# Optimization experiments

Hardware: AMD Instinct MI355X
Metric: run time of the kernel (lower is better)

Reference implementation:

```python
import jax, jax.numpy as jnp
import numpy as np

N = 50000          # nodes
E = 800000         # edges per metapath
M = 3              # metapaths
IN_DIM = 256
H = 8              # heads
D = 32             # out_dim per head
HID = 128          # semantic attention hidden
NEG_SLOPE = 0.2    # DGL GATConv default leaky_relu slope


def setup_inputs() -> dict:
    key = jax.random.key(0)
    ks = jax.random.split(key, 10)
    h = jax.random.normal(ks[0], (N, IN_DIM), dtype=jnp.float32)
    src = jax.random.randint(ks[1], (M, E), 0, N, dtype=jnp.int32)
    dst = jax.random.randint(ks[2], (M, E), 0, N, dtype=jnp.int32)
    s = 1.0 / np.sqrt(IN_DIM)
    fc_w = jax.random.normal(ks[3], (M, IN_DIM, H * D), dtype=jnp.float32) * s
    attn_l = jax.random.normal(ks[4], (M, H, D), dtype=jnp.float32) * 0.1
    attn_r = jax.random.normal(ks[5], (M, H, D), dtype=jnp.float32) * 0.1
    bias = jnp.zeros((M, H * D), dtype=jnp.float32)
    sem_w1 = jax.random.normal(ks[6], (H * D, HID), dtype=jnp.float32) * (1.0 / np.sqrt(H * D))
    sem_b1 = jnp.zeros((HID,), dtype=jnp.float32)
    sem_w2 = jax.random.normal(ks[7], (HID, 1), dtype=jnp.float32) * (1.0 / np.sqrt(HID))
    return {"h": h, "src": src, "dst": dst, "fc_w": fc_w, "attn_l": attn_l,
            "attn_r": attn_r, "bias": bias, "sem_w1": sem_w1, "sem_b1": sem_b1,
            "sem_w2": sem_w2}


def _gat(h, src, dst, fc_w, attn_l, attn_r, bias):
    # DGL GATConv (eval mode, dropout=0), activation=elu.
    feat = (h @ fc_w).reshape(N, H, D)                       # [N,H,D]
    el = jnp.sum(feat * attn_l, axis=-1)                     # [N,H]
    er = jnp.sum(feat * attn_r, axis=-1)                     # [N,H]
    e = jax.nn.leaky_relu(el[src] + er[dst], NEG_SLOPE)      # [E,H]
    # edge softmax over incoming edges of each dst node
    emax = jax.ops.segment_max(e, dst, num_segments=N)       # [N,H]
    emax = jnp.where(jnp.isfinite(emax), emax, 0.0)
    ee = jnp.exp(e - emax[dst])                              # [E,H]
    esum = jax.ops.segment_sum(ee, dst, num_segments=N)      # [N,H]
    alpha = ee / jnp.maximum(esum[dst], 1e-38)               # [E,H]
    msg = feat[src] * alpha[:, :, None]                      # [E,H,D]
    rst = jax.ops.segment_sum(msg, dst, num_segments=N)      # [N,H,D]
    rst = rst + bias.reshape(1, H, D)
    return jax.nn.elu(rst).reshape(N, H * D)                 # flatten heads


def reference(h, src, dst, fc_w, attn_l, attn_r, bias, sem_w1, sem_b1, sem_w2):
    gat_all = jax.vmap(_gat, in_axes=(None, 0, 0, 0, 0, 0, 0))
    z_m = gat_all(h, src, dst, fc_w, attn_l, attn_r, bias)   # [M,N,F]
    z_m = jnp.transpose(z_m, (1, 0, 2))                      # [N,M,F]
    # semantic attention
    w = jnp.tanh(z_m @ sem_w1 + sem_b1) @ sem_w2             # [N,M,1]
    w = w.mean(axis=0)                                       # [M,1]
    a_w = jax.nn.softmax(w, axis=0)                          # [M,1]
    z = jnp.sum(z_m * a_w[None, :, :], axis=1)               # [N,F]
    return z
```

## Files before the change

kernel.cpp:

```cpp
#include <hip/hip_runtime.h>
#include <math.h>

#define NN   50000
#define EE   800000
#define MM   3
#define KDIM 256
#define FF   256
#define HH   8
#define DD   32
#define HID  128
#define SLOPE 0.2f
#define BK   32
#define CAP  80

typedef unsigned short u16;
typedef unsigned int   u32;
typedef __attribute__((ext_vector_type(8))) short short8;
typedef __attribute__((ext_vector_type(4))) float floatx4;

__device__ __forceinline__ float eluf(float x) { return x > 0.f ? x : expm1f(x); }

__device__ __forceinline__ float b2f_lo(u32 u) {
    union { u32 i; float f; } v; v.i = u << 16; return v.f;
}
__device__ __forceinline__ float b2f_hi(u32 u) {
    union { u32 i; float f; } v; v.i = u & 0xffff0000u; return v.f;
}
__device__ __forceinline__ u16 f2b(float f) {
    union { float f; u32 i; } v; v.f = f;
    u32 lsb = (v.i >> 16) & 1u;
    v.i += 0x7fffu + lsb;
    return (u16)(v.i >> 16);
}
__device__ __forceinline__ u32 pack2(float lo, float hi) {
    return (u32)f2b(lo) | ((u32)f2b(hi) << 16);
}

__device__ __forceinline__ void gload_lds16(const u16* g, u16* l) {
    __builtin_amdgcn_global_load_lds(
        (const __attribute__((address_space(1))) unsigned int*)(const void*)g,
        (__attribute__((address_space(3))) unsigned int*)(void*)l,
        16, 0, 0);
}

__global__ __launch_bounds__(256) void k_prep(
    const float* __restrict__ hmat, u16* __restrict__ hb,
    const float* __restrict__ fcw,  u16* __restrict__ fcwt,
    const float* __restrict__ w1,   u16* __restrict__ w1t,
    int* __restrict__ cnt, float* __restrict__ wsum)
{
    const int bid = blockIdx.x;
    const int t = threadIdx.x;
    if (bid < 6250) {
        long long i = ((long long)bid * 256 + t) * 8;
        float4 v0 = *(const float4*)(hmat + i);
        float4 v1 = *(const float4*)(hmat + i + 4);
        uint4 u;
        u.x = pack2(v0.x, v0.y); u.y = pack2(v0.z, v0.w);
        u.z = pack2(v1.x, v1.y); u.w = pack2(v1.z, v1.w);
        *(uint4*)(hb + i) = u;
    } else if (bid < 7018) {
        int wb = bid - 6250;
        int k = wb & 255, me = wb >> 8, n = t;
        float v = fcw[((size_t)me * KDIM + k) * FF + n];
        fcwt[((size_t)me * FF + n) * KDIM + k] = f2b(v);
    } else if (bid < 7146) {
        int idx = (bid - 7018) * 256 + t;
        int k = idx >> 7, n = idx & 127;
        w1t[(size_t)n * KDIM + k] = f2b(w1[(size_t)k * HID + n]);
    } else if (bid < 7293) {
        int idx = (bid - 7146) * 256 + t;
        if (idx < (MM * NN) / 4)
            ((uint4*)cnt)[idx] = make_uint4(0u, 0u, 0u, 0u);
    } else {
        if (t < 16) ((uint4*)wsum)[t] = make_uint4(0u, 0u, 0u, 0u);
    }
}

__global__ __launch_bounds__(256) void k_feat_all(
    const u16*   __restrict__ hb,
    const u16*   __restrict__ fcwt,
    const float* __restrict__ al,
    const float* __restrict__ ar,
    u16*   __restrict__ featb,
    float* __restrict__ el,
    float* __restrict__ er,
    const int* __restrict__ src,
    const int* __restrict__ dst,
    int* __restrict__ cnt,
    u16* __restrict__ srt)
{
    __shared__ u16 As[128 * BK];
    __shared__ u16 Bs[128 * BK];

    const int t = threadIdx.x;

    {
        int bid = blockIdx.x + 391 * (blockIdx.y + 2 * blockIdx.z);
        long long base = ((long long)bid * 256 + t) * 4;
        if (base < (long long)MM * EE) {
            int4 d4 = *(const int4*)(dst + base);
            int4 s4 = *(const int4*)(src + base);
            int me = (int)(base / EE);
            int* cnt_m = cnt + (size_t)me * NN;
            u16* srt_m = srt + (size_t)me * CAP * NN;
            int dd4[4] = { d4.x, d4.y, d4.z, d4.w };
            int ss4[4] = { s4.x, s4.y, s4.z, s4.w };
            #pragma unroll
            for (int j = 0; j < 4; ++j) {
                int slot = atomicAdd(&cnt_m[dd4[j]], 1);
                if (slot < CAP) srt_m[(size_t)slot * NN + dd4[j]] = (u16)ss4[j];
            }
        }
    }

    const int n0 = blockIdx.x * 128;
    const int cy = blockIdx.y;
    const int m  = blockIdx.z;
    const int c_base = cy * 128;
    const int wave = t >> 6, lane = t & 63;
    const int wr = wave >> 1, wc = wave & 1;
    const int quad = lane >> 4, l15 = lane & 15;

    const u16* fcwt_m = fcwt + (size_t)m * FF * KDIM;
    const float* al_m = al + (size_t)m * HH * DD;
    const float* ar_m = ar + (size_t)m * HH * DD;

    const u16* pA[2]; const u16* pB[2]; u16* lA[2]; u16* lB[2];
    #pragma unroll
    for (int i = 0; i < 2; ++i) {
        int r  = wave * 32 + i * 16 + (lane >> 2);
        int cs = (((lane & 3) ^ (r & 3)) << 3);
        pA[i] = hb + (size_t)min(n0 + r, NN - 1) * KDIM + cs;
        pB[i] = fcwt_m + (size_t)(c_base + r) * KDIM + cs;
        lA[i] = (u16*)As + (wave * 2 + i) * 512;
        lB[i] = (u16*)Bs + (wave * 2 + i) * 512;
    }

    int aoff[4], boff[4];
    #pragma unroll
    for (int ti = 0; ti < 4; ++ti) {
        int rowa = wr * 64 + ti * 16 + l15;
        aoff[ti] = rowa * BK + (((quad ^ (rowa & 3))) << 3);
        int rowb = wc * 64 + ti * 16 + l15;
        boff[ti] = rowb * BK + (((quad ^ (rowb & 3))) << 3);
    }

    floatx4 acc[4][4] = {};

    for (int k0 = 0; k0 < KDIM; k0 += BK) {
        __syncthreads();
        #pragma unroll
        for (int i = 0; i < 2; ++i) {
            gload_lds16(pA[i] + k0, lA[i]);
            gload_lds16(pB[i] + k0, lB[i]);
        }
        __syncthreads();

        short8 afr[4], bfr[4];
        #pragma unroll
        for (int ti = 0; ti < 4; ++ti)
            afr[ti] = *(const short8*)(&As[aoff[ti]]);
        #pragma unroll
        for (int tj = 0; tj < 4; ++tj)
            bfr[tj] = *(const short8*)(&Bs[boff[tj]]);
        #pragma unroll
        for (int ti = 0; ti < 4; ++ti)
            #pragma unroll
            for (int tj = 0; tj < 4; ++tj)
                acc[ti][tj] = __builtin_amdgcn_mfma_f32_16x16x32_bf16(
                    afr[ti], bfr[tj], acc[ti][tj], 0, 0, 0);
    }

    float alv[4], arv[4];
    #pragma unroll
    for (int tj = 0; tj < 4; ++tj) {
        int h = cy * 4 + wc * 2 + (tj >> 1);
        int dcol = (tj & 1) * 16 + l15;
        alv[tj] = al_m[h * DD + dcol];
        arv[tj] = ar_m[h * DD + dcol];
    }
    const int h0 = cy * 4 + wc * 2, h1 = h0 + 1;

    #pragma unroll
    for (int ti = 0; ti < 4; ++ti) {
        #pragma unroll
        for (int reg = 0; reg < 4; ++reg) {
            int n = n0 + wr * 64 + ti * 16 + quad * 4 + reg;
            bool ok = n < NN;
            if (ok) {
                #pragma unroll
                for (int tj = 0; tj < 4; ++tj) {
                    int c = c_base + wc * 64 + tj * 16 + l15;
                    featb[((size_t)m * NN + n) * FF + c] = f2b(acc[ti][tj][reg]);
                }
            }
            float pl0 = acc[ti][0][reg] * alv[0] + acc[ti][1][reg] * alv[1];
            float pl1 = acc[ti][2][reg] * alv[2] + acc[ti][3][reg] * alv[3];
            float pr0 = acc[ti][0][reg] * arv[0] + acc[ti][1][reg] * arv[1];
            float pr1 = acc[ti][2][reg] * arv[2] + acc[ti][3][reg] * arv[3];
            #pragma unroll
            for (int s = 1; s < 16; s <<= 1) {
                pl0 += __shfl_xor(pl0, s); pl1 += __shfl_xor(pl1, s);
                pr0 += __shfl_xor(pr0, s); pr1 += __shfl_xor(pr1, s);
            }
            if (l15 == 0 && ok) {
                el[((size_t)m * NN + n) * HH + h0] = pl0;
                el[((size_t)m * NN + n) * HH + h1] = pl1;
                er[((size_t)m * NN + n) * HH + h0] = pr0;
                er[((size_t)m * NN + n) * HH + h1] = pr1;
            }
        }
    }
}

__global__ __launch_bounds__(256) void k_aggr_all(
    const int* __restrict__ cnt,
    const u16* __restrict__ srt,
    const float* __restrict__ el,
    const float* __restrict__ er,
    const u16* __restrict__ featb,
    const float* __restrict__ bias,
    u16* __restrict__ z)
{
    __shared__ float alpha_s[4][2][CAP][HH];
    __shared__ int   srcoff[4][2][CAP];

    const int m = blockIdx.y;
    const int wave = threadIdx.x >> 6, lane = threadIdx.x & 63;
    const int half = lane >> 5, L = lane & 31;
    const int d = blockIdx.x * 8 + wave * 2 + half;

    const int deg = min(cnt[(size_t)m * NN + d], CAP);
    const float* el_m = el + (size_t)m * NN * HH;
    const u16* feat_m = featb + (size_t)m * NN * FF;

    #pragma unroll
    for (int i = 0; i < 3; ++i) {
        int slot = L + i * 32;
        if (slot < deg)
            srcoff[wave][half][slot] =
                (int)srt[(size_t)(m * CAP + slot) * NN + d] * FF;
    }

    const int hA = L & 7;
    const float er_d = er[((size_t)m * NN + d) * HH + hA];
    float esum_r = 0.f;
    const int nIter = (deg + 3) >> 2;
    int i = 0;
    for (; i + 2 <= nIter; i += 2) {
        int j0 = i * 4 + (L >> 3);
        int j1 = j0 + 4;
        bool v0 = j0 < deg, v1 = j1 < deg;
        int so0 = v0 ? srcoff[wave][half][j0] : 0;
        int so1 = v1 ? srcoff[wave][half][j1] : 0;
        float x0 = el_m[(size_t)(so0 >> 5) + hA] + er_d;
        float x1 = el_m[(size_t)(so1 >> 5) + hA] + er_d;
        x0 = x0 >= 0.f ? x0 : SLOPE * x0;  x0 = fminf(x0, 60.f);
        x1 = x1 >= 0.f ? x1 : SLOPE * x1;  x1 = fminf(x1, 60.f);
        float e0 = v0 ? expf(x0) : 0.f;
        float e1 = v1 ? expf(x1) : 0.f;
        if (v0) alpha_s[wave][half][j0][hA] = e0;
        if (v1) alpha_s[wave][half][j1][hA] = e1;
        float g = e0 + e1;
        g += __shfl_xor(g, 8); g += __shfl_xor(g, 16);
        esum_r += g;
    }
    for (; i < nIter; ++i) {
        int j = i * 4 + (L >> 3);
        float e = 0.f;
        if (j < deg) {
            int so = srcoff[wave][half][j];
            float x = el_m[(size_t)(so >> 5) + hA] + er_d;
            x = x >= 0.f ? x : SLOPE * x;
            x = fminf(x, 60.f);
            e = expf(x);
            alpha_s[wave][half][j][hA] = e;
        }
        float g = e;
        g += __shfl_xor(g, 8); g += __shfl_xor(g, 16);
        esum_r += g;
    }
    float inv_r = 1.f / fmaxf(esum_r, 1e-38f);

    const float inv_g = __shfl(inv_r, (lane & 32) | (L >> 2));
    const int hB = L >> 2;
    const u16* frow = feat_m + L * 8;
    float acc[8] = {0.f, 0.f, 0.f, 0.f, 0.f, 0.f, 0.f, 0.f};

#define ACC8(f, a)                                                  \
    acc[0] += (a) * b2f_lo((f).x); acc[1] += (a) * b2f_hi((f).x);   \
    acc[2] += (a) * b2f_lo((f).y); acc[3] += (a) * b2f_hi((f).y);   \
    acc[4] += (a) * b2f_lo((f).z); acc[5] += (a) * b2f_hi((f).z);   \
    acc[6] += (a) * b2f_lo((f).w); acc[7] += (a) * b2f_hi((f).w);

    int j = 0;
    for (; j + 4 <= deg; j += 4) {
        int so0 = srcoff[wave][half][j + 0];
        int so1 = srcoff[wave][half][j + 1];
        int so2 = srcoff[wave][half][j + 2];
        int so3 = srcoff[wave][half][j + 3];
        float a0 = alpha_s[wave][half][j + 0][hB];
        float a1 = alpha_s[wave][half][j + 1][hB];
        float a2 = alpha_s[wave][half][j + 2][hB];
        float a3 = alpha_s[wave][half][j + 3][hB];
        uint4 f0 = *(const uint4*)(frow + so0);
        uint4 f1 = *(const uint4*)(frow + so1);
        uint4 f2 = *(const uint4*)(frow + so2);
        uint4 f3 = *(const uint4*)(frow + so3);
        ACC8(f0, a0); ACC8(f1, a1); ACC8(f2, a2); ACC8(f3, a3);
    }
    for (; j < deg; ++j) {
        int so = srcoff[wave][half][j];
        float a = alpha_s[wave][half][j][hB];
        uint4 f = *(const uint4*)(frow + so);
        ACC8(f, a);
    }
#undef ACC8

    #pragma unroll
    for (int k = 0; k < 8; ++k) acc[k] *= inv_g;

    const float4 b0 = *(const float4*)(bias + (size_t)m * FF + L * 8);
    const float4 b1 = *(const float4*)(bias + (size_t)m * FF + L * 8 + 4);
    uint4 o;
    o.x = pack2(eluf(acc[0] + b0.x), eluf(acc[1] + b0.y));
    o.y = pack2(eluf(acc[2] + b0.z), eluf(acc[3] + b0.w));
    o.z = pack2(eluf(acc[4] + b1.x), eluf(acc[5] + b1.y));
    o.w = pack2(eluf(acc[6] + b1.z), eluf(acc[7] + b1.w));
    *(uint4*)(z + ((size_t)m * NN + d) * FF + L * 8) = o;
}

__global__ __launch_bounds__(256) void k_sem_all(
    const u16* __restrict__ z,
    const u16* __restrict__ w1t,
    const float* __restrict__ b1,
    const float* __restrict__ w2,
    float* __restrict__ wsum)
{
    __shared__ u16 As[128 * BK];
    __shared__ u16 Bs[128 * BK];

    const int n0 = blockIdx.x * 128;
    const int m  = blockIdx.y;
    const int t = threadIdx.x;
    const int wave = t >> 6, lane = t & 63;
    const int wr = wave >> 1, wc = wave & 1;
    const int quad = lane >> 4, l15 = lane & 15;

    const u16* z_m = z + (size_t)m * NN * FF;

    const u16* pA[2]; const u16* pB[2]; u16* lA[2]; u16* lB[2];
    #pragma unroll
    for (int i = 0; i < 2; ++i) {
        int r  = wave * 32 + i * 16 + (lane >> 2);
        int cs = (((lane & 3) ^ (r & 3)) << 3);
        pA[i] = z_m + (size_t)min(n0 + r, NN - 1) * FF + cs;
        pB[i] = w1t + (size_t)r * KDIM + cs;
        lA[i] = (u16*)As + (wave * 2 + i) * 512;
        lB[i] = (u16*)Bs + (wave * 2 + i) * 512;
    }

    int aoff[4], boff[4];
    #pragma unroll
    for (int ti = 0; ti < 4; ++ti) {
        int rowa = wr * 64 + ti * 16 + l15;
        aoff[ti] = rowa * BK + (((quad ^ (rowa & 3))) << 3);
        int rowb = wc * 64 + ti * 16 + l15;
        boff[ti] = rowb * BK + (((quad ^ (rowb & 3))) << 3);
    }

    floatx4 acc[4][4] = {};

    for (int k0 = 0; k0 < KDIM; k0 += BK) {
        __syncthreads();
        #pragma unroll
        for (int i = 0; i < 2; ++i) {
            gload_lds16(pA[i] + k0, lA[i]);
            gload_lds16(pB[i] + k0, lB[i]);
        }
        __syncthreads();

        short8 afr[4], bfr[4];
        #pragma unroll
        for (int ti = 0; ti < 4; ++ti)
            afr[ti] = *(const short8*)(&As[aoff[ti]]);
        #pragma unroll
        for (int tj = 0; tj < 4; ++tj)
            bfr[tj] = *(const short8*)(&Bs[boff[tj]]);
        #pragma unroll
        for (int ti = 0; ti < 4; ++ti)
            #pragma unroll
            for (int tj = 0; tj < 4; ++tj)
                acc[ti][tj] = __builtin_amdgcn_mfma_f32_16x16x32_bf16(
                    afr[ti], bfr[tj], acc[ti][tj], 0, 0, 0);
    }

    float b1v[4], w2v[4];
    #pragma unroll
    for (int tj = 0; tj < 4; ++tj) {
        int c = wc * 64 + tj * 16 + l15;
        b1v[tj] = b1[c];
        w2v[tj] = w2[c];
    }
    float local = 0.f;
    #pragma unroll
    for (int ti = 0; ti < 4; ++ti) {
        #pragma unroll
        for (int reg = 0; reg < 4; ++reg) {
            int n = n0 + wr * 64 + ti * 16 + quad * 4 + reg;
            if (n < NN) {
                #pragma unroll
                for (int tj = 0; tj < 4; ++tj)
                    local += tanhf(acc[ti][tj][reg] + b1v[tj]) * w2v[tj];
            }
        }
    }
    #pragma unroll
    for (int s = 1; s < 64; s <<= 1) local += __shfl_xor(local, s);
    if (lane == 0) atomicAdd(&wsum[m], local);
}

__global__ __launch_bounds__(256) void k_combine(
    const u16* __restrict__ z, const float* __restrict__ wsum,
    float* __restrict__ out)
{
    float s0 = wsum[0] / (float)NN, s1 = wsum[1] / (float)NN, s2 = wsum[2] / (float)NN;
    float mx = fmaxf(s0, fmaxf(s1, s2));
    float e0 = expf(s0 - mx), e1 = expf(s1 - mx), e2 = expf(s2 - mx);
    float inv = 1.f / (e0 + e1 + e2);
    float aw[3] = { e0 * inv, e1 * inv, e2 * inv };

    long long idx = (long long)blockIdx.x * 256 + threadIdx.x;
    if (idx >= (long long)NN * 32) return;
    int n = (int)(idx >> 5), c = (int)(idx & 31) * 8;
    float acc[8] = {0.f, 0.f, 0.f, 0.f, 0.f, 0.f, 0.f, 0.f};
    #pragma unroll
    for (int m = 0; m < MM; ++m) {
        uint4 f = *(const uint4*)(z + ((size_t)m * NN + n) * FF + c);
        float a = aw[m];
        acc[0] += a * b2f_lo(f.x); acc[1] += a * b2f_hi(f.x);
        acc[2] += a * b2f_lo(f.y); acc[3] += a * b2f_hi(f.y);
        acc[4] += a * b2f_lo(f.z); acc[5] += a * b2f_hi(f.z);
        acc[6] += a * b2f_lo(f.w); acc[7] += a * b2f_hi(f.w);
    }
    float* op = out + (size_t)n * FF + c;
    *(float4*)op       = make_float4(acc[0], acc[1], acc[2], acc[3]);
    *(float4*)(op + 4) = make_float4(acc[4], acc[5], acc[6], acc[7]);
}

extern "C" void kernel_launch(void* const* d_in, const int* in_sizes, int n_in,
                              void* d_out, int out_size, void* d_ws, size_t ws_size,
                              hipStream_t stream)
{
    const float* hmat = (const float*)d_in[0];
    const int*   src  = (const int*)d_in[1];
    const int*   dst  = (const int*)d_in[2];
    const float* fcw  = (const float*)d_in[3];
    const float* al   = (const float*)d_in[4];
    const float* ar   = (const float*)d_in[5];
    const float* bias = (const float*)d_in[6];
    const float* w1   = (const float*)d_in[7];
    const float* b1   = (const float*)d_in[8];
    const float* w2   = (const float*)d_in[9];
    float* out = (float*)d_out;

    char* ws = (char*)d_ws;
    size_t off = 0;
    auto alloc = [&](size_t nbytes) {
        void* p = (void*)(ws + off);
        off = (off + nbytes + 255) & ~(size_t)255;
        return p;
    };
    float* el   = (float*)alloc((size_t)MM * NN * HH * 4);
    float* er   = (float*)alloc((size_t)MM * NN * HH * 4);
    float* wsum = (float*)alloc(256);
    int*   cnt  = (int*)alloc((size_t)MM * NN * 4);
    u16*   srt  = (u16*)alloc((size_t)MM * CAP * NN * 2);
    u16*   fcwt = (u16*)alloc((size_t)MM * KDIM * FF * 2);
    u16*   w1t  = (u16*)alloc((size_t)HID * KDIM * 2);
    u16*   hb   = (u16*)alloc((size_t)NN * KDIM * 2);
    u16*   featb= (u16*)alloc((size_t)MM * NN * FF * 2);
    u16*   z    = (u16*)alloc((size_t)MM * NN * FF * 2);

    k_prep<<<7294, 256, 0, stream>>>(hmat, hb, fcw, fcwt, w1, w1t, cnt, wsum);

    k_feat_all<<<dim3((NN + 127) / 128, 2, MM), 256, 0, stream>>>(
        hb, fcwt, al, ar, featb, el, er, src, dst, cnt, srt);

    k_aggr_all<<<dim3(NN / 8, MM), 256, 0, stream>>>(
        cnt, srt, el, er, featb, bias, z);
    k_sem_all<<<dim3((NN + 127) / 128, MM), 256, 0, stream>>>(z, w1t, b1, w2, wsum);
    k_combine<<<(int)(((size_t)NN * 32 + 255) / 256), 256, 0, stream>>>(z, wsum, out);
}
```

Before: 556.9 us.

## Preload full semantic weight into LDS and read A fragments directly from global

Result: no change. 559.2 us (+0.4%).

```diff
diff --git a/kernel.cpp b/kernel.cpp
--- a/kernel.cpp
+++ b/kernel.cpp
@@ -338,8 +338,7 @@
     const float* __restrict__ w2,
     float* __restrict__ wsum)
 {
-    __shared__ u16 As[128 * BK];
-    __shared__ u16 Bs[128 * BK];
+    __shared__ u16 Bs[HID * KDIM];
 
     const int n0 = blockIdx.x * 128;
     const int m  = blockIdx.y;
@@ -350,44 +349,40 @@
 
     const u16* z_m = z + (size_t)m * NN * FF;
 
-    const u16* pA[2]; const u16* pB[2]; u16* lA[2]; u16* lB[2];
-    #pragma unroll
-    for (int i = 0; i < 2; ++i) {
-        int r  = wave * 32 + i * 16 + (lane >> 2);
-        int cs = (((lane & 3) ^ (r & 3)) << 3);
-        pA[i] = z_m + (size_t)min(n0 + r, NN - 1) * FF + cs;
-        pB[i] = w1t + (size_t)r * KDIM + cs;
-        lA[i] = (u16*)As + (wave * 2 + i) * 512;
-        lB[i] = (u16*)Bs + (wave * 2 + i) * 512;
-    }
-
-    int aoff[4], boff[4];
+    #pragma unroll
+    for (int i = 0; i < 16; ++i) {
+        int flat = i * 256 + t;
+        int row = flat >> 5;
+        int g = (flat >> 2) & 7, s = flat & 3;
+        int col = g * 32 + (((s ^ (row & 3))) << 3);
+        gload_lds16(w1t + (size_t)row * KDIM + col, (u16*)Bs + (size_t)flat * 8);
+    }
+    __syncthreads();
+
+    const u16* pa[4];
     #pragma unroll
     for (int ti = 0; ti < 4; ++ti) {
-        int rowa = wr * 64 + ti * 16 + l15;
-        aoff[ti] = rowa * BK + (((quad ^ (rowa & 3))) << 3);
-        int rowb = wc * 64 + ti * 16 + l15;
-        boff[ti] = rowb * BK + (((quad ^ (rowb & 3))) << 3);
+        int n = min(n0 + wr * 64 + ti * 16 + l15, NN - 1);
+        pa[ti] = z_m + (size_t)n * FF + quad * 8;
+    }
+    int boff[4];
+    #pragma unroll
+    for (int tj = 0; tj < 4; ++tj) {
+        int row = wc * 64 + tj * 16 + l15;
+        boff[tj] = row * KDIM + (((quad ^ (row & 3))) << 3);
     }
 
     floatx4 acc[4][4] = {};
 
+    #pragma unroll
     for (int k0 = 0; k0 < KDIM; k0 += BK) {
-        __syncthreads();
-        #pragma unroll
-        for (int i = 0; i < 2; ++i) {
-            gload_lds16(pA[i] + k0, lA[i]);
-            gload_lds16(pB[i] + k0, lB[i]);
-        }
-        __syncthreads();
-
         short8 afr[4], bfr[4];
         #pragma unroll
         for (int ti = 0; ti < 4; ++ti)
-            afr[ti] = *(const short8*)(&As[aoff[ti]]);
+            afr[ti] = *(const short8*)(pa[ti] + k0);
         #pragma unroll
         for (int tj = 0; tj < 4; ++tj)
-            bfr[tj] = *(const short8*)(&Bs[boff[tj]]);
+            bfr[tj] = *(const short8*)(&Bs[boff[tj] + k0]);
         #pragma unroll
         for (int ti = 0; ti < 4; ++ti)
             #pragma unroll
```
